# Performance work log

Measured on AMD Instinct MI355X. Metric: run time of the kernel, lower is better.

## Reference

```python
import jax, jax.numpy as jnp
from jax import lax
import numpy as np

PATCH = 8
THRESHOLD = 0.2  # learned per-layer threshold, at init value


def conv2d(x, w, b, pad):
    # x: (N,C,H,W), w: (O,I,kh,kw)
    y = lax.conv_general_dilated(x, w, (1, 1), [(pad, pad), (pad, pad)],
                                 dimension_numbers=('NCHW', 'OIHW', 'NCHW'))
    return y + b[None, :, None, None]


def extract_patches(X, p):
    # Appends 4 positional channels, then splits into non-overlapping p x p patches.
    B, C, H, W = X.shape
    gy, gx = jnp.meshgrid(jnp.linspace(0.0, 1.0, H), jnp.linspace(0.0, 1.0, W), indexing='ij')
    pos = jnp.stack([gx, gy, jnp.sin(jnp.pi * gx), jnp.sin(jnp.pi * gy)]).astype(X.dtype)  # (4,H,W)
    Xc = jnp.concatenate([X, jnp.broadcast_to(pos[None], (B, 4, H, W))], axis=1)  # (B,C+4,H,W)
    h, w = H // p, W // p
    Xp = Xc.reshape(B, C + 4, h, p, w, p).transpose(0, 2, 4, 1, 3, 5).reshape(B, h * w, C + 4, p, p)
    return Xp, h, w


def _forward(X,
             proj_w0, proj_b0, exp_w0, exp_b0, fin_w0, fin_b0,
             proj_w1, proj_b1, exp_w1, exp_b1, fin_w1, fin_b1,
             proj_w2, proj_b2, exp_w2, exp_b2, fin_w2, fin_b2,
             proj_w3, proj_b3, exp_w3, exp_b3, fin_w3, fin_b3,
             router_w, router_b, lin_w, lin_b):
    layers = [
        (proj_w0, proj_b0, exp_w0, exp_b0, fin_w0, fin_b0),
        (proj_w1, proj_b1, exp_w1, exp_b1, fin_w1, fin_b1),
        (proj_w2, proj_b2, exp_w2, exp_b2, fin_w2, fin_b2),
        (proj_w3, proj_b3, exp_w3, exp_b3, fin_w3, fin_b3),
    ]
    for (pw, pb, ew, eb, fw, fb) in layers:
        Xp, h, w = extract_patches(X, PATCH)        # (B,P,C,p,p)
        B, P, C, pH, pW = Xp.shape
        flat = Xp.reshape(B * P, C, pH, pW)
        # router: conv-proj -> global avg pool -> linear -> softmax
        pooled = conv2d(flat, pw, pb, 1).mean(axis=(2, 3))                 # (BP, 8)
        scores = jax.nn.softmax(pooled @ router_w.T + router_b, axis=-1)  # (BP, E)
        scores = scores.reshape(B, P, -1)                                  # (B,P,E)
        # all experts as one grouped conv: (E,Co,C,3,3) -> (E*Co,C,3,3)
        E, Co = ew.shape[0], ew.shape[1]
        eo = conv2d(flat, ew.reshape(E * Co, C, 3, 3), eb.reshape(E * Co), 1)
        eo = jax.nn.relu(eo).reshape(B, P, E, Co, pH, pW)
        # expert is skipped unless some patch score exceeds the layer threshold
        gate = (scores.max(axis=(0, 1)) > THRESHOLD).astype(X.dtype)        # (E,)
        comb = jnp.einsum('bpechw,bpe->bpchw', eo, scores * gate[None, None, :])
        img = comb.reshape(B, h, w, Co, pH, pW).transpose(0, 3, 1, 4, 2, 5)
        img = img.reshape(B, Co, h * pH, w * pW)
        X = conv2d(img, fw, fb, 4)  # 1x1 conv, padding=4 -> H,W grow by 8
    return X.reshape(X.shape[0], -1) @ lin_w.T + lin_b


def setup_inputs() -> dict:
    key = jax.random.key(0)
    ks = iter(jax.random.split(key, 64))

    def nrm(shape, fan_in):
        return jax.random.normal(next(ks), shape, jnp.float32) / np.sqrt(fan_in)

    d = {"X": jax.random.normal(next(ks), (16, 3, 64, 64), jnp.float32)}
    cin = [7, 68, 68, 132]   # expert/key input channels per layer (prev out + 4 pos)
    cout = [64, 64, 128, 128]
    E = 4
    for l in range(4):
        d[f"proj_w{l}"] = nrm((8, cin[l], 3, 3), cin[l] * 9)
        d[f"proj_b{l}"] = jnp.zeros((8,), jnp.float32)
        d[f"exp_w{l}"] = nrm((E, cout[l], cin[l], 3, 3), cin[l] * 9)
        d[f"exp_b{l}"] = jnp.zeros((E, cout[l]), jnp.float32)
        d[f"fin_w{l}"] = nrm((cout[l], cout[l], 1, 1), cout[l])
        d[f"fin_b{l}"] = jnp.zeros((cout[l],), jnp.float32)
    d["router_w"] = nrm((E, 8), 8)
    d["router_b"] = jnp.zeros((E,), jnp.float32)
    feat = 128 * 96 * 96  # final (B,128,96,96) flattened
    d["lin_w"] = nrm((10, feat), feat)
    d["lin_b"] = jnp.zeros((10,), jnp.float32)
    return d


def reference(X,
              proj_w0, proj_b0, exp_w0, exp_b0, fin_w0, fin_b0,
              proj_w1, proj_b1, exp_w1, exp_b1, fin_w1, fin_b1,
              proj_w2, proj_b2, exp_w2, exp_b2, fin_w2, fin_b2,
              proj_w3, proj_b3, exp_w3, exp_b3, fin_w3, fin_b3,
              router_w, router_b, lin_w, lin_b):
    return _forward(X,
                    proj_w0, proj_b0, exp_w0, exp_b0, fin_w0, fin_b0,
                    proj_w1, proj_b1, exp_w1, exp_b1, fin_w1, fin_b1,
                    proj_w2, proj_b2, exp_w2, exp_b2, fin_w2, fin_b2,
                    proj_w3, proj_b3, exp_w3, exp_b3, fin_w3, fin_b3,
                    router_w, router_b, lin_w, lin_b)
```

## Files before the change

kernel.cpp:

```cpp
#include <hip/hip_runtime.h>
#include <math.h>

#define NB 16
#define NE 4
#define THRESH 0.2f
#define LIN_NS 64

typedef __attribute__((ext_vector_type(8))) _Float16 f16x8;
typedef __attribute__((ext_vector_type(4))) float f32x4;
typedef unsigned short u16;
typedef unsigned int u32;

__device__ inline u16 f16bits(float v) { _Float16 h = (_Float16)v; return __builtin_bit_cast(u16, h); }

__global__ void repack_all_kernel(const float* __restrict__ ew, const float* __restrict__ fw,
    u16* __restrict__ Wm, u16* __restrict__ Wp, u16* __restrict__ fW,
    int CO, int CIN, int CINp, int C) {
    const int M = NE * CO;
    const int n1 = 9 * M * CINp, n2 = M * 64, n3 = CO * CO;
    const int n = n1 + n2 + n3;
    for (int i = blockIdx.x * blockDim.x + threadIdx.x; i < n; i += gridDim.x * blockDim.x) {
        if (i < n1) {
            int k = i % CINp; int t = i / CINp; int m = t % M; int ij = t / M;
            float v = (k < CIN) ? ew[(m * C + k) * 9 + ij] : 0.f;
            Wm[i] = f16bits(v);
        } else if (i < n1 + n2) {
            int j = i - n1; int kp = j & 63; int m = j >> 6;
            float v = 0.f;
            if (kp < 36) { int pc = kp / 9, ij = kp % 9; v = ew[(m * C + CIN + pc) * 9 + ij]; }
            Wp[j] = f16bits(v);
        } else {
            int j = i - n1 - n2;
            fW[j] = f16bits(fw[j]);
        }
    }
}

template<int CIN, int C>
__global__ __launch_bounds__(256) void router_kernel(
    const float* __restrict__ X, const float* __restrict__ pw, const float* __restrict__ pb,
    const float* __restrict__ rw, const float* __restrict__ rb,
    float* __restrict__ scores, int H, int W, int nP)
{
    __shared__ float S[4][C * 9 + 8];
    const int wv = threadIdx.x >> 6;
    const int lane = threadIdx.x & 63;
    const int bp = blockIdx.x * 4 + wv;
    const int P = nP * nP;
    const int b = bp / P, pi = bp % P;
    const int py = pi / nP, px = pi % nP;
    const int h = lane >> 3, w = lane & 7;
    const int gy = py * 8 + h, gx = px * 8 + w;
    float* Sw = S[wv];
    for (int c = 0; c < C; ++c) {
        float v;
        if (c < CIN) {
            v = X[(((size_t)b * CIN + c) * H + gy) * W + gx];
        } else {
            float t = (c == CIN || c == CIN + 2) ? gx * (1.f / (W - 1)) : gy * (1.f / (H - 1));
            v = (c >= CIN + 2) ? sinf(3.14159265358979323846f * t) : t;
        }
        float r = v;
        r += __shfl_xor(r, 1); r += __shfl_xor(r, 2); r += __shfl_xor(r, 4);
        float cc = v;
        cc += __shfl_xor(cc, 8); cc += __shfl_xor(cc, 16); cc += __shfl_xor(cc, 32);
        float T = r;
        T += __shfl_xor(T, 8); T += __shfl_xor(T, 16); T += __shfl_xor(T, 32);
        float R0 = __shfl(r, 0), R7 = __shfl(r, 56);
        float C0 = __shfl(cc, 0), C7 = __shfl(cc, 7);
        float x00 = __shfl(v, 0), x07 = __shfl(v, 7);
        float x70 = __shfl(v, 56), x77 = __shfl(v, 63);
        if (lane < 9) {
            int i = lane / 3, j = lane % 3;
            float s = T;
            if (i == 0) s -= R7; else if (i == 2) s -= R0;
            if (j == 0) s -= C7; else if (j == 2) s -= C0;
            if (i == 0 && j == 0) s += x77;
            else if (i == 0 && j == 2) s += x70;
            else if (i == 2 && j == 0) s += x07;
            else if (i == 2 && j == 2) s += x00;
            Sw[c * 9 + lane] = s;
        }
    }
    __syncthreads();
    if (lane < 8) {
        const int o = lane;
        float acc = 0.f;
        for (int c = 0; c < C; ++c) {
            #pragma unroll
            for (int ij = 0; ij < 9; ++ij)
                acc += pw[(o * C + c) * 9 + ij] * Sw[c * 9 + ij];
        }
        Sw[C * 9 + o] = acc * (1.f / 64.f) + pb[o];
    }
    __syncthreads();
    if (lane == 0) {
        float lg[NE];
        float m = -1e30f;
        #pragma unroll
        for (int e = 0; e < NE; ++e) {
            float a = rb[e];
            #pragma unroll
            for (int o = 0; o < 8; ++o) a += Sw[C * 9 + o] * rw[e * 8 + o];
            lg[e] = a;
            m = fmaxf(m, a);
        }
        float ssum = 0.f;
        #pragma unroll
        for (int e = 0; e < NE; ++e) { lg[e] = __expf(lg[e] - m); ssum += lg[e]; }
        float inv = 1.f / ssum;
        #pragma unroll
        for (int e = 0; e < NE; ++e) scores[bp * NE + e] = lg[e] * inv;
    }
}

__global__ __launch_bounds__(256) void gate_kernel(const float* __restrict__ scores, int BP,
                                                   float* __restrict__ gate)
{
    __shared__ float sm[4][NE];
    float m[NE] = {-1e30f, -1e30f, -1e30f, -1e30f};
    for (int i = threadIdx.x; i < BP; i += 256) {
        #pragma unroll
        for (int e = 0; e < NE; ++e) m[e] = fmaxf(m[e], scores[i * NE + e]);
    }
    #pragma unroll
    for (int e = 0; e < NE; ++e) {
        float v = m[e];
        for (int o = 32; o; o >>= 1) v = fmaxf(v, __shfl_xor(v, o));
        m[e] = v;
    }
    int wv = threadIdx.x >> 6, lane = threadIdx.x & 63;
    if (lane == 0) {
        #pragma unroll
        for (int e = 0; e < NE; ++e) sm[wv][e] = m[e];
    }
    __syncthreads();
    if (threadIdx.x == 0) {
        #pragma unroll
        for (int e = 0; e < NE; ++e) {
            float mx = fmaxf(fmaxf(sm[0][e], sm[1][e]), fmaxf(sm[2][e], sm[3][e]));
            gate[e] = (mx > THRESH) ? 1.f : 0.f;
        }
    }
}

__global__ __launch_bounds__(256) void border_kernel(float* __restrict__ Xn,
                                                     const float* __restrict__ fb,
                                                     int CO, int H, int W)
{
    const int Hout = H + 8, Wout = W + 8;
    const int nb = 16 * H + 64;
    const long total = (long)NB * CO * nb;
    for (long i = (long)blockIdx.x * blockDim.x + threadIdx.x; i < total;
         i += (long)gridDim.x * blockDim.x) {
        int j = (int)(i % nb); long t = i / nb; int o = (int)(t % CO); int b = (int)(t / CO);
        int y, x;
        if (j < 4 * Wout)       { y = j / Wout;             x = j % Wout; }
        else if (j < 8 * Wout)  { int j2 = j - 4 * Wout; y = H + 4 + j2 / Wout; x = j2 % Wout; }
        else                    { int j3 = j - 8 * Wout; y = 4 + j3 / 8;
                                  int c8 = j3 % 8; x = (c8 < 4) ? c8 : W + 4 + (c8 - 4); }
        Xn[(((size_t)b * CO + o) * Hout + y) * Wout + x] = fb[o];
    }
}

template<int CIN, int CINp, int CO>
__global__ __launch_bounds__(512, 2) void expert_fused_kernel(
    const float* __restrict__ X,
    const u16* __restrict__ Wm, const u16* __restrict__ Wp, const u16* __restrict__ fW,
    const float* __restrict__ eb, const float* __restrict__ fb,
    const float* __restrict__ scores, const float* __restrict__ gate,
    float* __restrict__ Xn, int H, int W, int nP)
{
    constexpr int M = NE * CO;
    constexpr int KSM = CINp / 32;
    constexpr int SP = CINp + 8;
    constexpr int PIP = 72;
    constexpr int CP = CO + 8;
    constexpr bool FAT = (CO == 128);
    constexpr int NT = FAT ? 8 : 4;
    constexpr int PATW = 2 * 100 * SP;
    constexpr int POSW = 2 * 64 * PIP;
    constexpr int COMBW = 2 * 64 * CP;
    constexpr int SMW = (PATW + POSW > COMBW) ? (PATW + POSW) : COMBW;

    __shared__ __align__(16) u16 smem[SMW];
    __shared__ float pospix[2][4][64];
    u16* pat = smem;
    u16* posim = smem + PATW;
    u16* comb = smem;

    const int P = nP * nP;
    const int bp0 = blockIdx.x * 2, bp1 = bp0 + 1;
    const int b0 = bp0 / P, pi0 = bp0 % P, py0 = pi0 / nP, px0 = pi0 % nP;
    const int b1 = bp1 / P, pi1 = bp1 % P, py1 = pi1 / nP, px1 = pi1 % nP;
    const int tid = threadIdx.x;
    const int Hout = H + 8, Wout = W + 8;

    for (int i = tid; i < 100 * SP; i += 512) ((u32*)pat)[i] = 0;
    {
        int g = tid >> 8, r = tid & 255, pc = r >> 6, p = r & 63;
        int gy = (g ? py1 : py0) * 8 + (p >> 3), gx = (g ? px1 : px0) * 8 + (p & 7);
        float t = (pc == 0 || pc == 2) ? gx * (1.f / (W - 1)) : gy * (1.f / (H - 1));
        pospix[g][pc][p] = (pc >= 2) ? sinf(3.14159265358979323846f * t) : t;
    }
    __syncthreads();
    for (int i = tid; i < 2 * CIN * 16; i += 512) {
        int g = i / (CIN * 16), j = i % (CIN * 16);
        int c = j >> 4, q = j & 15, h = q >> 1, w4 = (q & 1) * 4;
        int bb = g ? b1 : b0, py = g ? py1 : py0, px = g ? px1 : px0;
        const float4 v = *(const float4*)&X[(((size_t)bb * CIN + c) * H + py * 8 + h) * W + px * 8 + w4];
        int base = g * 100 * SP + c;
        pat[base + ((h + 1) * 10 + (w4 + 1)) * SP] = f16bits(v.x);
        pat[base + ((h + 1) * 10 + (w4 + 2)) * SP] = f16bits(v.y);
        pat[base + ((h + 1) * 10 + (w4 + 3)) * SP] = f16bits(v.z);
        pat[base + ((h + 1) * 10 + (w4 + 4)) * SP] = f16bits(v.w);
    }
    for (int i = tid; i < 2 * 64 * 64; i += 512) {
        int g = i >> 12, r = i & 4095, pix = r >> 6, kp = r & 63;
        float v = 0.f;
        if (kp < 36) {
            int pc = kp / 9, ij = kp % 9;
            int hh = (pix >> 3) + ij / 3 - 1, ww = (pix & 7) + ij % 3 - 1;
            if (hh >= 0 && hh < 8 && ww >= 0 && ww < 8) v = pospix[g][pc][hh * 8 + ww];
        }
        posim[g * 64 * PIP + pix * PIP + kp] = f16bits(v);
    }
    __syncthreads();

    const int lane = tid & 63, wv = tid >> 6;
    const int colp = lane & 15, kg = lane >> 4;
    const int cot = FAT ? wv : (wv & 3);
    const int gO = FAT ? 0 : (wv >> 2);
    const int co0 = cot * 16;

    int prow[NT];
    #pragma unroll
    for (int nt = 0; nt < NT; ++nt) {
        int g = FAT ? (nt >> 2) : gO;
        int pix = (nt & 3) * 16 + colp;
        prow[nt] = g * 100 * SP + ((pix >> 3) * 10 + (pix & 7)) * SP;
    }
    int aoff[NE];
    #pragma unroll
    for (int e = 0; e < NE; ++e)
        aoff[e] = (e * CO + co0 + colp) * CINp + kg * 8;

    f32x4 acc[NE][NT];
    #pragma unroll
    for (int e = 0; e < NE; ++e)
        #pragma unroll
        for (int nt = 0; nt < NT; ++nt) acc[e][nt] = (f32x4){0.f, 0.f, 0.f, 0.f};

    for (int ij = 0; ij < 9; ++ij) {
        const int tap = (ij / 3) * 10 + (ij % 3);
        const int wb = ij * M * CINp;
        #pragma unroll
        for (int ks = 0; ks < KSM; ++ks) {
            f16x8 Bv[NT];
            #pragma unroll
            for (int nt = 0; nt < NT; ++nt)
                Bv[nt] = *(const f16x8*)&pat[prow[nt] + tap * SP + ks * 32 + kg * 8];
            #pragma unroll
            for (int e = 0; e < NE; ++e) {
                f16x8 Ah = *(const f16x8*)(Wm + wb + aoff[e] + ks * 32);
                __builtin_amdgcn_s_setprio(1);
                #pragma unroll
                for (int nt = 0; nt < NT; ++nt)
                    acc[e][nt] = __builtin_amdgcn_mfma_f32_16x16x32_f16(Ah, Bv[nt], acc[e][nt], 0, 0, 0);
                __builtin_amdgcn_s_setprio(0);
            }
        }
    }
    #pragma unroll
    for (int ks = 0; ks < 2; ++ks) {
        f16x8 Bv[NT];
        #pragma unroll
        for (int nt = 0; nt < NT; ++nt) {
            int g = FAT ? (nt >> 2) : gO;
            int pix = (nt & 3) * 16 + colp;
            Bv[nt] = *(const f16x8*)&posim[g * 64 * PIP + pix * PIP + ks * 32 + kg * 8];
        }
        #pragma unroll
        for (int e = 0; e < NE; ++e) {
            int ao = (e * CO + co0 + colp) * 64 + ks * 32 + kg * 8;
            f16x8 Ah = *(const f16x8*)(Wp + ao);
            __builtin_amdgcn_s_setprio(1);
            #pragma unroll
            for (int nt = 0; nt < NT; ++nt)
                acc[e][nt] = __builtin_amdgcn_mfma_f32_16x16x32_f16(Ah, Bv[nt], acc[e][nt], 0, 0, 0);
            __builtin_amdgcn_s_setprio(0);
        }
    }

    float sg0[NE], sg1[NE];
    #pragma unroll
    for (int e = 0; e < NE; ++e) {
        float gv = gate[e];
        sg0[e] = scores[bp0 * NE + e] * gv;
        sg1[e] = scores[bp1 * NE + e] * gv;
    }
    float ebv[NE][4];
    #pragma unroll
    for (int e = 0; e < NE; ++e)
        #pragma unroll
        for (int r = 0; r < 4; ++r) ebv[e][r] = eb[e * CO + co0 + kg * 4 + r];

    __syncthreads();

    #pragma unroll
    for (int nt = 0; nt < NT; ++nt) {
        const int g = FAT ? (nt >> 2) : gO;
        int pix = (nt & 3) * 16 + colp;
        u16 hv[4];
        #pragma unroll
        for (int r = 0; r < 4; ++r) {
            float cv = 0.f;
            #pragma unroll
            for (int e = 0; e < NE; ++e) {
                float s = g ? sg1[e] : sg0[e];
                cv += s * fmaxf(acc[e][nt][r] + ebv[e][r], 0.f);
            }
            hv[r] = f16bits(cv);
        }
        uint2 q;
        q.x = (u32)hv[0] | ((u32)hv[1] << 16);
        q.y = (u32)hv[2] | ((u32)hv[3] << 16);
        *(uint2*)&comb[g * 64 * CP + pix * CP + co0 + kg * 4] = q;
    }
    __syncthreads();

    const int o0 = co0;
    f32x4 accF[NT];
    #pragma unroll
    for (int nt = 0; nt < NT; ++nt) accF[nt] = (f32x4){0.f, 0.f, 0.f, 0.f};
    #pragma unroll
    for (int ks = 0; ks < CO / 32; ++ks) {
        int ao = (o0 + colp) * CO + ks * 32 + kg * 8;
        f16x8 ah = *(const f16x8*)(fW + ao);
        __builtin_amdgcn_s_setprio(1);
        #pragma unroll
        for (int nt = 0; nt < NT; ++nt) {
            int g = FAT ? (nt >> 2) : gO;
            int pix = (nt & 3) * 16 + colp;
            f16x8 bv = *(const f16x8*)&comb[g * 64 * CP + pix * CP + ks * 32 + kg * 8];
            accF[nt] = __builtin_amdgcn_mfma_f32_16x16x32_f16(ah, bv, accF[nt], 0, 0, 0);
        }
        __builtin_amdgcn_s_setprio(0);
    }
    float fbv[4];
    #pragma unroll
    for (int r = 0; r < 4; ++r) fbv[r] = fb[o0 + kg * 4 + r];
    #pragma unroll
    for (int nt = 0; nt < NT; ++nt) {
        const int g = FAT ? (nt >> 2) : gO;
        int pix = (nt & 3) * 16 + colp;
        int bb = g ? b1 : b0, py = g ? py1 : py0, px = g ? px1 : px0;
        int gy = py * 8 + (pix >> 3) + 4, gx = px * 8 + (pix & 7) + 4;
        #pragma unroll
        for (int r = 0; r < 4; ++r) {
            int o = o0 + kg * 4 + r;
            Xn[(((size_t)bb * CO + o) * Hout + gy) * Wout + gx] = accF[nt][r] + fbv[r];
        }
    }
}

__global__ __launch_bounds__(256) void linear_part_kernel(
    const float* __restrict__ Xf, const float* __restrict__ lw, float* __restrict__ part)
{
    const int feat = 128 * 96 * 96;
    const int CH = feat / LIN_NS;
    const int b = blockIdx.x / LIN_NS, s = blockIdx.x % LIN_NS;
    const float4* xa = (const float4*)(Xf + (size_t)b * feat + (size_t)s * CH);
    const float* wbase = lw + (size_t)s * CH;
    float acc[10];
    #pragma unroll
    for (int o = 0; o < 10; ++o) acc[o] = 0.f;
    const int n4 = CH / 4;
    for (int i = threadIdx.x; i < n4; i += 256) {
        float4 xv = xa[i];
        #pragma unroll
        for (int o = 0; o < 10; ++o) {
            float4 wv = *(const float4*)(wbase + (size_t)o * feat + i * 4);
            acc[o] += xv.x * wv.x + xv.y * wv.y + xv.z * wv.z + xv.w * wv.w;
        }
    }
    #pragma unroll
    for (int o = 0; o < 10; ++o)
        for (int m = 32; m; m >>= 1) acc[o] += __shfl_xor(acc[o], m);
    __shared__ float sm[4][10];
    int wv = threadIdx.x >> 6, lane = threadIdx.x & 63;
    if (lane == 0) {
        #pragma unroll
        for (int o = 0; o < 10; ++o) sm[wv][o] = acc[o];
    }
    __syncthreads();
    if (threadIdx.x < 10)
        part[(b * LIN_NS + s) * 10 + threadIdx.x] =
            sm[0][threadIdx.x] + sm[1][threadIdx.x] + sm[2][threadIdx.x] + sm[3][threadIdx.x];
}

__global__ __launch_bounds__(256) void linear_reduce_kernel(
    const float* __restrict__ part, const float* __restrict__ lb, float* __restrict__ out)
{
    int i = threadIdx.x;
    if (i < 160) {
        int b = i / 10, o = i % 10;
        float a = lb[o];
        for (int s = 0; s < LIN_NS; ++s) a += part[(b * LIN_NS + s) * 10 + o];
        out[i] = a;
    }
}

template<int CIN, int CINp, int CO>
static void run_layer(const float* Xin, int H, int nP, const float* const* Lw,
                      const float* rw, const float* rb,
                      u16* Wm, u16* Wp, u16* fW,
                      float* scores, float* gate, float* Xn, hipStream_t stream)
{
    const int W = H;
    const int BP = NB * nP * nP;
    const float* pw = Lw[0]; const float* pb = Lw[1];
    const float* ew = Lw[2]; const float* ebias = Lw[3];
    const float* fw = Lw[4]; const float* fb = Lw[5];

    repack_all_kernel<<<1024, 256, 0, stream>>>(ew, fw, Wm, Wp, fW, CO, CIN, CINp, CIN + 4);
    router_kernel<CIN, CIN + 4><<<BP / 4, 256, 0, stream>>>(Xin, pw, pb, rw, rb, scores, H, W, nP);
    gate_kernel<<<1, 256, 0, stream>>>(scores, BP, gate);
    border_kernel<<<2048, 256, 0, stream>>>(Xn, fb, CO, H, W);
    expert_fused_kernel<CIN, CINp, CO><<<BP / 2, 512, 0, stream>>>(
        Xin, Wm, Wp, fW, ebias, fb, scores, gate, Xn, H, W, nP);
}

extern "C" void kernel_launch(void* const* d_in, const int* in_sizes, int n_in,
                              void* d_out, int out_size, void* d_ws, size_t ws_size,
                              hipStream_t stream)
{
    const float* X0 = (const float*)d_in[0];
    const float* L[4][6];
    for (int l = 0; l < 4; ++l)
        for (int k = 0; k < 6; ++k) L[l][k] = (const float*)d_in[1 + l * 6 + k];
    const float* rw = (const float*)d_in[25];
    const float* rb = (const float*)d_in[26];
    const float* lw = (const float*)d_in[27];
    const float* lb = (const float*)d_in[28];

    char* ws = (char*)d_ws;
    const size_t XA_B = 63438848;
    const size_t XB_B = 75497472;
    const size_t WM_B = 1179648;
    const size_t WP_B = 65536;
    const size_t FW_B = 32768;
    float* XA = (float*)(ws);
    float* XB = (float*)(ws + XA_B);
    u16* Wm = (u16*)(ws + XA_B + XB_B);
    u16* Wp = (u16*)(ws + XA_B + XB_B + WM_B);
    u16* fW = (u16*)(ws + XA_B + XB_B + WM_B + WP_B);
    float* scores = (float*)(ws + XA_B + XB_B + WM_B + WP_B + FW_B);
    float* gate = scores + 1936 * 4;
    float* lpart = gate + 64;

    run_layer<3,   32,  64>(X0, 64,  8, L[0], rw, rb, Wm, Wp, fW, scores, gate, XA, stream);
    run_layer<64,  64,  64>(XA, 72,  9, L[1], rw, rb, Wm, Wp, fW, scores, gate, XB, stream);
    run_layer<64,  64, 128>(XB, 80, 10, L[2], rw, rb, Wm, Wp, fW, scores, gate, XA, stream);
    run_layer<128, 128, 128>(XA, 88, 11, L[3], rw, rb, Wm, Wp, fW, scores, gate, XB, stream);

    linear_part_kernel<<<16 * LIN_NS, 256, 0, stream>>>(XB, lw, lpart);
    linear_reduce_kernel<<<1, 256, 0, stream>>>(lpart, lb, (float*)d_out);
}
```

Baseline: 867.3 us.

## Split expert accumulation into passes to cut registers and raise occupancy

The expert MFMA loop now processes experts in passes (two experts at a time for the 128-channel layers), and partial combined results are kept as packed fp16 between passes. This shrinks the live accumulator set so launch bounds can request 4 blocks per CU instead of 2, aiming to improve latency hiding. The price is reloading patch B-fragments per pass, plus an extra fp16 rounding of partial sums. Weight repacking is also hoisted into one upfront set of launches with per-layer buffers, removing the serialization between repack and compute within each layer.

```diff
diff --git a/kernel.cpp b/kernel.cpp
--- a/kernel.cpp
+++ b/kernel.cpp
@@ -12,6 +12,10 @@
 typedef unsigned int u32;
 
 __device__ inline u16 f16bits(float v) { _Float16 h = (_Float16)v; return __builtin_bit_cast(u16, h); }
+__device__ inline u32 pack2(float a, float b) { return (u32)f16bits(a) | ((u32)f16bits(b) << 16); }
+__device__ inline float unpk(u32 x, int hi) {
+    return (float)__builtin_bit_cast(_Float16, (u16)(hi ? (x >> 16) : (x & 0xffff)));
+}
 
 __global__ void repack_all_kernel(const float* __restrict__ ew, const float* __restrict__ fw,
     u16* __restrict__ Wm, u16* __restrict__ Wp, u16* __restrict__ fW,
@@ -164,7 +168,7 @@
 }
 
 template<int CIN, int CINp, int CO>
-__global__ __launch_bounds__(512, 2) void expert_fused_kernel(
+__global__ __launch_bounds__(512, 4) void expert_fused_kernel(
     const float* __restrict__ X,
     const u16* __restrict__ Wm, const u16* __restrict__ Wp, const u16* __restrict__ fW,
     const float* __restrict__ eb, const float* __restrict__ fb,
@@ -178,6 +182,8 @@
     constexpr int CP = CO + 8;
     constexpr bool FAT = (CO == 128);
     constexpr int NT = FAT ? 8 : 4;
+    constexpr int EPP = FAT ? 2 : 4;
+    constexpr int NPASS = NE / EPP;
     constexpr int PATW = 2 * 100 * SP;
     constexpr int POSW = 2 * 64 * PIP;
     constexpr int COMBW = 2 * 64 * CP;
@@ -240,70 +246,91 @@
         int pix = (nt & 3) * 16 + colp;
         prow[nt] = g * 100 * SP + ((pix >> 3) * 10 + (pix & 7)) * SP;
     }
-    int aoff[NE];
-    #pragma unroll
-    for (int e = 0; e < NE; ++e)
-        aoff[e] = (e * CO + co0 + colp) * CINp + kg * 8;
-
-    f32x4 acc[NE][NT];
-    #pragma unroll
-    for (int e = 0; e < NE; ++e)
-        #pragma unroll
-        for (int nt = 0; nt < NT; ++nt) acc[e][nt] = (f32x4){0.f, 0.f, 0.f, 0.f};
-
-    for (int ij = 0; ij < 9; ++ij) {
-        const int tap = (ij / 3) * 10 + (ij % 3);
-        const int wb = ij * M * CINp;
-        #pragma unroll
-        for (int ks = 0; ks < KSM; ++ks) {
-            f16x8 Bv[NT];
-            #pragma unroll
-            for (int nt = 0; nt < NT; ++nt)
-                Bv[nt] = *(const f16x8*)&pat[prow[nt] + tap * SP + ks * 32 + kg * 8];
-            #pragma unroll
-            for (int e = 0; e < NE; ++e) {
-                f16x8 Ah = *(const f16x8*)(Wm + wb + aoff[e] + ks * 32);
+
+    u32 pk[NT][2];
+
+    #pragma unroll
+    for (int pass = 0; pass < NPASS; ++pass) {
+        f32x4 acc[EPP][NT];
+        #pragma unroll
+        for (int ee = 0; ee < EPP; ++ee)
+            #pragma unroll
+            for (int nt = 0; nt < NT; ++nt) acc[ee][nt] = (f32x4){0.f, 0.f, 0.f, 0.f};
+
+        int aoff[EPP];
+        #pragma unroll
+        for (int ee = 0; ee < EPP; ++ee)
+            aoff[ee] = ((pass * EPP + ee) * CO + co0 + colp) * CINp + kg * 8;
+
+        for (int ij = 0; ij < 9; ++ij) {
+            const int tap = (ij / 3) * 10 + (ij % 3);
+            const int wb = ij * M * CINp;
+            #pragma unroll
+            for (int ks = 0; ks < KSM; ++ks) {
+                f16x8 Ah[EPP];
+                #pragma unroll
+                for (int ee = 0; ee < EPP; ++ee)
+                    Ah[ee] = *(const f16x8*)(Wm + wb + aoff[ee] + ks * 32);
                 __builtin_amdgcn_s_setprio(1);
                 #pragma unroll
-                for (int nt = 0; nt < NT; ++nt)
-                    acc[e][nt] = __builtin_amdgcn_mfma_f32_16x16x32_f16(Ah, Bv[nt], acc[e][nt], 0, 0, 0);
+                for (int nt = 0; nt < NT; ++nt) {
+                    f16x8 Bv = *(const f16x8*)&pat[prow[nt] + tap * SP + ks * 32 + kg * 8];
+                    #pragma unroll
+                    for (int ee = 0; ee < EPP; ++ee)
+                        acc[ee][nt] = __builtin_amdgcn_mfma_f32_16x16x32_f16(Ah[ee], Bv, acc[ee][nt], 0, 0, 0);
+                }
                 __builtin_amdgcn_s_setprio(0);
             }
         }
-    }
-    #pragma unroll
-    for (int ks = 0; ks < 2; ++ks) {
-        f16x8 Bv[NT];
+        #pragma unroll
+        for (int ks = 0; ks < 2; ++ks) {
+            f16x8 Ah[EPP];
+            #pragma unroll
+            for (int ee = 0; ee < EPP; ++ee)
+                Ah[ee] = *(const f16x8*)(Wp + ((pass * EPP + ee) * CO + co0 + colp) * 64 + ks * 32 + kg * 8);
+            __builtin_amdgcn_s_setprio(1);
+            #pragma unroll
+            for (int nt = 0; nt < NT; ++nt) {
+                int g = FAT ? (nt >> 2) : gO;
+                int pix = (nt & 3) * 16 + colp;
+                f16x8 Bv = *(const f16x8*)&posim[g * 64 * PIP + pix * PIP + ks * 32 + kg * 8];
+                #pragma unroll
+                for (int ee = 0; ee < EPP; ++ee)
+                    acc[ee][nt] = __builtin_amdgcn_mfma_f32_16x16x32_f16(Ah[ee], Bv, acc[ee][nt], 0, 0, 0);
+            }
+            __builtin_amdgcn_s_setprio(0);
+        }
+
+        float sgA[2][EPP], ebvP[EPP][4];
+        #pragma unroll
+        for (int ee = 0; ee < EPP; ++ee) {
+            int e = pass * EPP + ee;
+            float gv = gate[e];
+            sgA[0][ee] = scores[bp0 * NE + e] * gv;
+            sgA[1][ee] = scores[bp1 * NE + e] * gv;
+            #pragma unroll
+            for (int r = 0; r < 4; ++r) ebvP[ee][r] = eb[e * CO + co0 + kg * 4 + r];
+        }
         #pragma unroll
         for (int nt = 0; nt < NT; ++nt) {
-            int g = FAT ? (nt >> 2) : gO;
-            int pix = (nt & 3) * 16 + colp;
-            Bv[nt] = *(const f16x8*)&posim[g * 64 * PIP + pix * PIP + ks * 32 + kg * 8];
-        }
-        #pragma unroll
-        for (int e = 0; e < NE; ++e) {
-            int ao = (e * CO + co0 + colp) * 64 + ks * 32 + kg * 8;
-            f16x8 Ah = *(const f16x8*)(Wp + ao);
-            __builtin_amdgcn_s_setprio(1);
-            #pragma unroll
-            for (int nt = 0; nt < NT; ++nt)
-                acc[e][nt] = __builtin_amdgcn_mfma_f32_16x16x32_f16(Ah, Bv[nt], acc[e][nt], 0, 0, 0);
-            __builtin_amdgcn_s_setprio(0);
-        }
-    }
-
-    float sg0[NE], sg1[NE];
-    #pragma unroll
-    for (int e = 0; e < NE; ++e) {
-        float gv = gate[e];
-        sg0[e] = scores[bp0 * NE + e] * gv;
-        sg1[e] = scores[bp1 * NE + e] * gv;
-    }
-    float ebv[NE][4];
-    #pragma unroll
-    for (int e = 0; e < NE; ++e)
-        #pragma unroll
-        for (int r = 0; r < 4; ++r) ebv[e][r] = eb[e * CO + co0 + kg * 4 + r];
+            const int g = FAT ? (nt >> 2) : gO;
+            #pragma unroll
+            for (int rr = 0; rr < 2; ++rr) {
+                float cv0 = 0.f, cv1 = 0.f;
+                #pragma unroll
+                for (int ee = 0; ee < EPP; ++ee) {
+                    float s = sgA[g][ee];
+                    cv0 += s * fmaxf(acc[ee][nt][2 * rr]     + ebvP[ee][2 * rr],     0.f);
+                    cv1 += s * fmaxf(acc[ee][nt][2 * rr + 1] + ebvP[ee][2 * rr + 1], 0.f);
+                }
+                if (NPASS == 2 && pass == 1) {
+                    cv0 += unpk(pk[nt][rr], 0);
+                    cv1 += unpk(pk[nt][rr], 1);
+                }
+                pk[nt][rr] = pack2(cv0, cv1);
+            }
+        }
+    }
 
     __syncthreads();
 
@@ -311,20 +338,9 @@
     for (int nt = 0; nt < NT; ++nt) {
         const int g = FAT ? (nt >> 2) : gO;
         int pix = (nt & 3) * 16 + colp;
-        u16 hv[4];
-        #pragma unroll
-        for (int r = 0; r < 4; ++r) {
-            float cv = 0.f;
-            #pragma unroll
-            for (int e = 0; e < NE; ++e) {
-                float s = g ? sg1[e] : sg0[e];
-                cv += s * fmaxf(acc[e][nt][r] + ebv[e][r], 0.f);
-            }
-            hv[r] = f16bits(cv);
-        }
         uint2 q;
-        q.x = (u32)hv[0] | ((u32)hv[1] << 16);
-        q.y = (u32)hv[2] | ((u32)hv[3] << 16);
+        q.x = pk[nt][0];
+        q.y = pk[nt][1];
         *(uint2*)&comb[g * 64 * CP + pix * CP + co0 + kg * 4] = q;
     }
     __syncthreads();
@@ -414,16 +430,15 @@
 template<int CIN, int CINp, int CO>
 static void run_layer(const float* Xin, int H, int nP, const float* const* Lw,
                       const float* rw, const float* rb,
-                      u16* Wm, u16* Wp, u16* fW,
+                      const u16* Wm, const u16* Wp, const u16* fW,
                       float* scores, float* gate, float* Xn, hipStream_t stream)
 {
     const int W = H;
     const int BP = NB * nP * nP;
     const float* pw = Lw[0]; const float* pb = Lw[1];
-    const float* ew = Lw[2]; const float* ebias = Lw[3];
-    const float* fw = Lw[4]; const float* fb = Lw[5];
-
-    repack_all_kernel<<<1024, 256, 0, stream>>>(ew, fw, Wm, Wp, fW, CO, CIN, CINp, CIN + 4);
+    const float* ebias = Lw[3];
+    const float* fb = Lw[5];
+
     router_kernel<CIN, CIN + 4><<<BP / 4, 256, 0, stream>>>(Xin, pw, pb, rw, rb, scores, H, W, nP);
     gate_kernel<<<1, 256, 0, stream>>>(scores, BP, gate);
     border_kernel<<<2048, 256, 0, stream>>>(Xn, fb, CO, H, W);
@@ -447,22 +462,31 @@
     char* ws = (char*)d_ws;
     const size_t XA_B = 63438848;
     const size_t XB_B = 75497472;
-    const size_t WM_B = 1179648;
-    const size_t WP_B = 65536;
-    const size_t FW_B = 32768;
     float* XA = (float*)(ws);
     float* XB = (float*)(ws + XA_B);
-    u16* Wm = (u16*)(ws + XA_B + XB_B);
-    u16* Wp = (u16*)(ws + XA_B + XB_B + WM_B);
-    u16* fW = (u16*)(ws + XA_B + XB_B + WM_B + WP_B);
-    float* scores = (float*)(ws + XA_B + XB_B + WM_B + WP_B + FW_B);
+    char* wp = ws + XA_B + XB_B;
+    const int cfg_CO[4]   = {64, 64, 128, 128};
+    const int cfg_CINp[4] = {32, 64, 64, 128};
+    u16 *Wm[4], *Wp[4], *fW[4];
+    for (int l = 0; l < 4; ++l) {
+        int M = NE * cfg_CO[l];
+        Wm[l] = (u16*)wp;            wp += (size_t)9 * M * cfg_CINp[l] * 2;
+        Wp[l] = (u16*)wp;            wp += (size_t)M * 64 * 2;
+        fW[l] = (u16*)wp;            wp += (size_t)cfg_CO[l] * cfg_CO[l] * 2;
+    }
+    float* scores = (float*)wp;
     float* gate = scores + 1936 * 4;
     float* lpart = gate + 64;
 
-    run_layer<3,   32,  64>(X0, 64,  8, L[0], rw, rb, Wm, Wp, fW, scores, gate, XA, stream);
-    run_layer<64,  64,  64>(XA, 72,  9, L[1], rw, rb, Wm, Wp, fW, scores, gate, XB, stream);
-    run_layer<64,  64, 128>(XB, 80, 10, L[2], rw, rb, Wm, Wp, fW, scores, gate, XA, stream);
-    run_layer<128, 128, 128>(XA, 88, 11, L[3], rw, rb, Wm, Wp, fW, scores, gate, XB, stream);
+    const int cfg_CIN[4] = {3, 64, 64, 128};
+    for (int l = 0; l < 4; ++l)
+        repack_all_kernel<<<512, 256, 0, stream>>>(L[l][2], L[l][4], Wm[l], Wp[l], fW[l],
+                                                   cfg_CO[l], cfg_CIN[l], cfg_CINp[l], cfg_CIN[l] + 4);
+
+    run_layer<3,   32,  64>(X0, 64,  8, L[0], rw, rb, Wm[0], Wp[0], fW[0], scores, gate, XA, stream);
+    run_layer<64,  64,  64>(XA, 72,  9, L[1], rw, rb, Wm[1], Wp[1], fW[1], scores, gate, XB, stream);
+    run_layer<64,  64, 128>(XB, 80, 10, L[2], rw, rb, Wm[2], Wp[2], fW[2], scores, gate, XA, stream);
+    run_layer<128, 128, 128>(XA, 88, 11, L[3], rw, rb, Wm[3], Wp[3], fW[3], scores, gate, XB, stream);
 
     linear_part_kernel<<<16 * LIN_NS, 256, 0, stream>>>(XB, lw, lpart);
     linear_reduce_kernel<<<1, 256, 0, stream>>>(lpart, lb, (float*)d_out);
```

New measurement: 841.7 us. 1.03x faster.
